# Optimization experiments

Measured on AMD Instinct MI355X. Metric: run time of the kernel, lower is better.

Reference implementation:

```python
import jax, jax.numpy as jnp
import numpy as np

N, E = 50000, 800000
F_NODE, F_EDGE, H, LAT, MAXN = 128, 16, 128, 64, 200


def setup_inputs() -> dict:
    key = jax.random.key(0)
    ks = jax.random.split(key, 40)
    s = 0.05
    p = {
        'x': jax.random.normal(ks[0], (N, F_NODE), jnp.float32),
        'edge_index': jax.random.randint(ks[1], (2, E), 0, N, jnp.int64),
        'edge_attr': jax.random.normal(ks[2], (E, F_EDGE), jnp.float32),
        'eps': jax.random.normal(ks[3], (1, LAT), jnp.float32),
        'num_nodes': N,
        # GATConv layer 1 (heads=1)
        'W1': jax.random.normal(ks[4], (F_NODE, H), jnp.float32) * s,
        'att_src1': jax.random.normal(ks[5], (H,), jnp.float32) * s,
        'att_dst1': jax.random.normal(ks[6], (H,), jnp.float32) * s,
        'We1': jax.random.normal(ks[7], (F_EDGE, H), jnp.float32) * s,
        'att_e1': jax.random.normal(ks[8], (H,), jnp.float32) * s,
        'b1': jnp.zeros((H,), jnp.float32),
        # GATConv layer 2
        'W2': jax.random.normal(ks[9], (H, H), jnp.float32) * s,
        'att_src2': jax.random.normal(ks[10], (H,), jnp.float32) * s,
        'att_dst2': jax.random.normal(ks[11], (H,), jnp.float32) * s,
        'We2': jax.random.normal(ks[12], (F_EDGE, H), jnp.float32) * s,
        'att_e2': jax.random.normal(ks[13], (H,), jnp.float32) * s,
        'b2': jnp.zeros((H,), jnp.float32),
        # heads
        'mu_W': jax.random.normal(ks[14], (H, LAT), jnp.float32) * s,
        'mu_b': jnp.zeros((LAT,), jnp.float32),
        'lv_W': jax.random.normal(ks[15], (H, LAT), jnp.float32) * s,
        'lv_b': jnp.zeros((LAT,), jnp.float32),
        'dec_W': jax.random.normal(ks[16], (LAT, H), jnp.float32) * s,
        'dec_b': jnp.zeros((H,), jnp.float32),
        'adj_W1': jax.random.normal(ks[17], (H, H), jnp.float32) * s,
        'adj_b1': jnp.zeros((H,), jnp.float32),
        'adj_W2': jax.random.normal(ks[18], (H, MAXN), jnp.float32) * s,
        'adj_b2': jnp.zeros((MAXN,), jnp.float32),
        'nd_W1': jax.random.normal(ks[19], (H, H), jnp.float32) * s,
        'nd_b1': jnp.zeros((H,), jnp.float32),
        'nd_W2': jax.random.normal(ks[20], (H, F_NODE), jnp.float32) * s,
        'nd_b2': jnp.zeros((F_NODE,), jnp.float32),
    }
    return p


def _gat(h, src, dst, ea, W, a_s, a_d, We, a_e, b, n):
    # PyG GATConv, heads=1: linear transform, per-edge attention, segment softmax over dst
    g = h @ W                                     # [n, H]
    alpha = jax.nn.leaky_relu((g @ a_s)[src] + (g @ a_d)[dst] + (ea @ We) @ a_e,
                              negative_slope=0.2)  # [E']
    m = jax.ops.segment_max(alpha, dst, num_segments=n)
    ex = jnp.exp(alpha - m[dst])
    den = jax.ops.segment_sum(ex, dst, num_segments=n)
    w = ex / den[dst]
    return jax.ops.segment_sum(w[:, None] * g[src], dst, num_segments=n) + b


def _forward(x, edge_index, edge_attr, eps, num_nodes,
             W1, att_src1, att_dst1, We1, att_e1, b1,
             W2, att_src2, att_dst2, We2, att_e2, b2,
             mu_W, mu_b, lv_W, lv_b, dec_W, dec_b,
             adj_W1, adj_b1, adj_W2, adj_b2, nd_W1, nd_b1, nd_W2, nd_b2):
    n = x.shape[0]
    src, dst = edge_index[0], edge_index[1]
    # add self loops; self-loop edge_attr = per-node mean of incoming edge_attr (PyG fill_value='mean')
    deg = jax.ops.segment_sum(jnp.ones((src.shape[0],), x.dtype), dst, num_segments=n)
    mean_ea = jax.ops.segment_sum(edge_attr, dst, num_segments=n) / jnp.maximum(deg, 1.0)[:, None]
    loop = jnp.arange(n)
    src_f = jnp.concatenate([src, loop])
    dst_f = jnp.concatenate([dst, loop])
    ea_f = jnp.concatenate([edge_attr, mean_ea])
    h = jax.nn.relu(_gat(x, src_f, dst_f, ea_f, W1, att_src1, att_dst1, We1, att_e1, b1, n))
    h = jax.nn.relu(_gat(h, src_f, dst_f, ea_f, W2, att_src2, att_dst2, We2, att_e2, b2, n))
    hg = h.mean(axis=0, keepdims=True)            # global_mean_pool, single graph -> [1, H]
    mu = hg @ mu_W + mu_b
    logvar = hg @ lv_W + lv_b
    z = mu + eps * jnp.exp(0.5 * logvar)
    hd = jax.nn.relu(z @ dec_W + dec_b)           # [1, H]
    hn = jnp.broadcast_to(hd[:, None, :], (1, num_nodes, hd.shape[-1]))
    adj = jax.nn.relu(hn @ adj_W1 + adj_b1) @ adj_W2 + adj_b2   # [1, n, MAXN]
    adj = adj[:, :, :num_nodes]
    nodes = jax.nn.relu(hn @ nd_W1 + nd_b1) @ nd_W2 + nd_b2     # [1, n, F_NODE]
    return adj, nodes, mu, logvar


def reference(x, edge_index, edge_attr, eps, num_nodes,
              W1, att_src1, att_dst1, We1, att_e1, b1,
              W2, att_src2, att_dst2, We2, att_e2, b2,
              mu_W, mu_b, lv_W, lv_b, dec_W, dec_b,
              adj_W1, adj_b1, adj_W2, adj_b2, nd_W1, nd_b1, nd_W2, nd_b2):
    return _forward(x, edge_index, edge_attr, eps, num_nodes,
                    W1, att_src1, att_dst1, We1, att_e1, b1,
                    W2, att_src2, att_dst2, We2, att_e2, b2,
                    mu_W, mu_b, lv_W, lv_b, dec_W, dec_b,
                    adj_W1, adj_b1, adj_W2, adj_b2, nd_W1, nd_b1, nd_W2, nd_b2)
```

## Files before the change

### kernel.cpp

```cpp
#include <hip/hip_runtime.h>
#include <math.h>

#define NN   50000
#define EE   800000
#define EF   850000
#define HH   128
#define FE   16
#define LATD 64
#define MAXNN 200

#define ADJ_TOT   10000000
#define NODES_TOT 6400000
#define OUT_TOT   16400000
#define MU_OFF    16400000
#define LV_OFF    16400064

#define GEMMBLOCKS 782
#define DEGBLOCKS  782
#define NBSCAN     49

typedef __attribute__((ext_vector_type(8))) short bf16x8;
typedef __attribute__((ext_vector_type(4))) float f32x4;
typedef __attribute__((ext_vector_type(2))) float f32x2;

__device__ __forceinline__ unsigned short f2bf(float f){
  unsigned int u = __float_as_uint(f);
  unsigned int r = (u + 0x7FFFu + ((u>>16)&1u)) >> 16;
  return (unsigned short)r;
}
__device__ __forceinline__ float bf2f(unsigned short h){
  return __uint_as_float(((unsigned int)h)<<16);
}

__device__ __forceinline__ void load_bo(const int* __restrict__ blocksum, int* bo, int tid){
  if(tid < 64){
    int v = (tid < NBSCAN)? blocksum[tid] : 0;
    int inc = v;
    #pragma unroll
    for(int off=1; off<64; off<<=1){
      int x = __shfl_up(inc, off);
      if(tid>=off) inc += x;
    }
    bo[tid] = inc - v;
  }
  __syncthreads();
}

__global__ __launch_bounds__(256) void kprep(int* ideg, float* hgsum,
                       const float* We1, const float* ae1, const float* We2, const float* ae2,
                       float* wa1, float* wa2,
                       const float* W1, const float* W2,
                       unsigned short* Wp1, unsigned short* Wp2){
  int i = blockIdx.x*256 + threadIdx.x;
  if(i < NN) ideg[i]=0;
  if(i < HH) hgsum[i]=0.f;
  if(i < FE){
    float s1=0.f, s2=0.f;
    for(int j=0;j<HH;j++){ s1 += We1[i*HH+j]*ae1[j]; s2 += We2[i*HH+j]*ae2[j]; }
    wa1[i]=s1; wa2[i]=s2;
  }
  if(i < HH*HH){
    int n = i >> 7, k = i & 127;
    Wp1[i] = f2bf(W1[k*HH + n]);
    Wp2[i] = f2bf(W2[k*HH + n]);
  }
}

__device__ __forceinline__ void gemm_body(int bid, int tid, const void* __restrict__ hin, int h_is_fp32,
    const unsigned short* __restrict__ Wp,
    const float* __restrict__ atts, const float* __restrict__ attd,
    unsigned char* __restrict__ A8, float* __restrict__ asrc, float* __restrict__ adst){
  int lane = tid & 63;
  int wid  = tid >> 6;
  int l = lane & 15, q = lane >> 4;
  int r0 = bid*64 + wid*16;
  if(r0 >= NN) return;
  const unsigned short* hb = (const unsigned short*)hin;
  const float*          hf = (const float*)hin;
  int row = r0 + l;

  bf16x8 afr[4];
  if(h_is_fp32){
    float4 u[8];
    #pragma unroll
    for(int kb=0;kb<4;kb++){
      const float* p = hf + (size_t)row*HH + kb*32 + q*8;
      u[kb*2]   = *(const float4*)(p);
      u[kb*2+1] = *(const float4*)(p+4);
    }
    #pragma unroll
    for(int kb=0;kb<4;kb++){
      afr[kb][0]=(short)f2bf(u[kb*2].x);   afr[kb][1]=(short)f2bf(u[kb*2].y);
      afr[kb][2]=(short)f2bf(u[kb*2].z);   afr[kb][3]=(short)f2bf(u[kb*2].w);
      afr[kb][4]=(short)f2bf(u[kb*2+1].x); afr[kb][5]=(short)f2bf(u[kb*2+1].y);
      afr[kb][6]=(short)f2bf(u[kb*2+1].z); afr[kb][7]=(short)f2bf(u[kb*2+1].w);
    }
  } else {
    #pragma unroll
    for(int kb=0;kb<4;kb++)
      afr[kb] = *(const bf16x8*)(hb + (size_t)row*HH + kb*32 + q*8);
  }

  f32x4 acc[8];
  #pragma unroll
  for(int t=0;t<8;t++) acc[t]=(f32x4){0.f,0.f,0.f,0.f};

  #pragma unroll
  for(int kb=0;kb<4;kb++){
    #pragma unroll
    for(int t=0;t<8;t++){
      bf16x8 b = *(const bf16x8*)(Wp + (size_t)(t*16+l)*HH + kb*32 + q*8);
      acc[t] = __builtin_amdgcn_mfma_f32_16x16x32_bf16(afr[kb], b, acc[t], 0,0,0);
    }
  }

  float av[8], dv[8];
  #pragma unroll
  for(int t=0;t<8;t++){ av[t]=atts[t*16+l]; dv[t]=attd[t*16+l]; }
  #pragma unroll
  for(int reg=0;reg<4;reg++){
    float ps=0.f, pd=0.f;
    #pragma unroll
    for(int t=0;t<8;t++){ ps+=acc[t][reg]*av[t]; pd+=acc[t][reg]*dv[t]; }
    #pragma unroll
    for(int m=8;m>=1;m>>=1){ ps+=__shfl_xor(ps,m,16); pd+=__shfl_xor(pd,m,16); }
    if(l==0){ int R=r0+q*4+reg; asrc[R]=ps; adst[R]=pd; }
  }
  #pragma unroll
  for(int t=0;t<8;t++)
    #pragma unroll
    for(int reg=0;reg<4;reg++){
      int pk = __builtin_amdgcn_cvt_pk_fp8_f32(acc[t][reg], 0.f, 0, false);
      A8[(size_t)(r0+q*4+reg)*HH + t*16 + l] = (unsigned char)(pk & 0xFF);
    }
}

__global__ __launch_bounds__(256) void kgemm3(const void* __restrict__ hin, int h_is_fp32,
    const unsigned short* __restrict__ Wp,
    const float* __restrict__ atts, const float* __restrict__ attd,
    unsigned char* __restrict__ A8, float* __restrict__ asrc, float* __restrict__ adst){
  gemm_body(blockIdx.x, threadIdx.x, hin, h_is_fp32, Wp, atts, attd, A8, asrc, adst);
}

__global__ __launch_bounds__(256) void kdeggemm(
    const int* __restrict__ ei, int* ideg, unsigned short* __restrict__ erank,
    const void* __restrict__ hin, int h_is_fp32,
    const unsigned short* __restrict__ Wp,
    const float* __restrict__ atts, const float* __restrict__ attd,
    unsigned char* __restrict__ A8, float* __restrict__ asrc, float* __restrict__ adst){
  if(blockIdx.x < GEMMBLOCKS){
    gemm_body(blockIdx.x, threadIdx.x, hin, h_is_fp32, Wp, atts, attd, A8, asrc, adst);
  } else {
    int e0 = ((blockIdx.x - GEMMBLOCKS)*256 + threadIdx.x)*4;
    if(e0 + 3 < EE){
      int4 d4 = *(const int4*)(ei + EE + e0);
      unsigned short r0 = (unsigned short)atomicAdd(&ideg[d4.x], 1);
      unsigned short r1 = (unsigned short)atomicAdd(&ideg[d4.y], 1);
      unsigned short r2 = (unsigned short)atomicAdd(&ideg[d4.z], 1);
      unsigned short r3 = (unsigned short)atomicAdd(&ideg[d4.w], 1);
      ushort4 rr; rr.x=r0; rr.y=r1; rr.z=r2; rr.w=r3;
      *(ushort4*)(erank + e0) = rr;
    } else {
      for(int j=0;j<4;j++)
        if(e0+j < EE) erank[e0+j] = (unsigned short)atomicAdd(&ideg[ei[EE+e0+j]], 1);
    }
  }
}

__global__ void kscan1(const int* __restrict__ ideg, int* rowstart, int* blocksum){
  __shared__ int sd[1024];
  int t=threadIdx.x; int i=blockIdx.x*1024+t;
  int v = (i<NN)? (ideg[i]+1) : 0;
  sd[t]=v; __syncthreads();
  for(int off=1; off<1024; off<<=1){
    int x = (t>=off)? sd[t-off] : 0;
    __syncthreads();
    sd[t] += x;
    __syncthreads();
  }
  if(i<NN) rowstart[i] = sd[t]-v;
  else if(i==NN) rowstart[NN] = sd[t];
  if(t==1023) blocksum[blockIdx.x]=sd[1023];
}

__device__ __forceinline__ unsigned etpack(const float4* a4,
                         const float* __restrict__ wa1, const float* __restrict__ wa2){
  float4 v0=a4[0], v1=a4[1], v2=a4[2], v3=a4[3];
  float va[16]={v0.x,v0.y,v0.z,v0.w, v1.x,v1.y,v1.z,v1.w,
                v2.x,v2.y,v2.z,v2.w, v3.x,v3.y,v3.z,v3.w};
  float d1=0.f,d2=0.f;
  #pragma unroll
  for(int f=0;f<FE;f++){ d1+=va[f]*wa1[f]; d2+=va[f]*wa2[f]; }
  return (unsigned)f2bf(d1) | ((unsigned)f2bf(d2)<<16);
}
__global__ __launch_bounds__(256) void kscatter(const int* __restrict__ ei, const float* __restrict__ ea,
                         const float* __restrict__ wa1, const float* __restrict__ wa2,
                         const int* __restrict__ rowstart, const int* __restrict__ blocksum,
                         const unsigned short* __restrict__ erank,
                         uint2* __restrict__ csr){
  __shared__ int bo[64];
  load_bo(blocksum, bo, threadIdx.x);
  int e0 = (blockIdx.x*256 + threadIdx.x)*2;
  if(e0>=EE) return;
  int sA=ei[e0],    sB=ei[e0+1];
  int dA=ei[EE+e0], dB=ei[EE+e0+1];
  int rA=(int)erank[e0], rB=(int)erank[e0+1];
  int pA=rowstart[dA]+bo[dA>>10]+rA, pB=rowstart[dB]+bo[dB>>10]+rB;
  const float4* a4 = (const float4*)(ea + (size_t)e0*FE);
  unsigned yA = etpack(a4,   wa1, wa2);
  unsigned yB = etpack(a4+4, wa1, wa2);
  uint2 enA; enA.x=(unsigned)sA; enA.y=yA;
  uint2 enB; enB.x=(unsigned)sB; enB.y=yB;
  csr[pA]=enA; csr[pB]=enB;
}

__global__ __launch_bounds__(256) void kgat(const unsigned char* __restrict__ A8,
    const float* __restrict__ asrc, const float* __restrict__ adst,
    const int* __restrict__ rowstart, const int* __restrict__ blocksum,
    const uint2* __restrict__ csr,
    int etsel, const float* __restrict__ bias,
    float* __restrict__ alphabuf, int* __restrict__ srcbuf,
    unsigned short* __restrict__ Bout){
  __shared__ int bo[64];
  load_bo(blocksum, bo, threadIdx.x);
  int lane = threadIdx.x & 63;
  int wid  = threadIdx.x >> 6;
  int i = blockIdx.x*4 + wid;
  if(i >= NN) return;
  int base = rowstart[i]   + bo[i>>10];
  int end  = rowstart[i+1] + bo[(i+1)>>10];
  int len  = end - base;
  float adi = adst[i];
  int lq = lane & 15;
  int qq = lane >> 4;
  float av[8];
  #pragma unroll
  for(int j=0;j<8;j++) av[j]=0.f;

  if(__builtin_expect(len <= 64, 1)){
    int s = i; float et = 0.f;
    if(lane < len-1){
      uint2 en = csr[base+lane];
      s = (int)en.x;
      et = etsel ? bf2f((unsigned short)(en.y>>16)) : bf2f((unsigned short)(en.y & 0xFFFFu));
    }
    float ets = (lane < len-1) ? et : 0.f;
    #pragma unroll
    for(int mk=32;mk>=1;mk>>=1) ets += __shfl_xor(ets,mk);
    if(lane == len-1) et = ets / fmaxf((float)(len-1), 1.f);
    float a = -1e30f;
    if(lane < len){
      a = asrc[s] + adi + et;
      a = fmaxf(a, 0.2f*a);
    }
    float m = a;
    #pragma unroll
    for(int mk=32;mk>=1;mk>>=1) m = fmaxf(m, __shfl_xor(m,mk));
    float ex = (lane<len) ? __expf(a-m) : 0.f;
    float sm = ex;
    #pragma unroll
    for(int mk=32;mk>=1;mk>>=1) sm += __shfl_xor(sm,mk);
    ex *= __builtin_amdgcn_rcpf(sm);

    int P4 = (len+3)>>2;
    for(int t0=0; t0<P4; t0+=6){
      int skv[6]; float w[6];
      #pragma unroll
      for(int j=0;j<6;j++){
        if(t0+j < P4){
          int idx = 4*(t0+j) + qq;
          skv[j] = __shfl(s, idx);
          w[j]   = __shfl(ex, idx);
        } else { skv[j] = i; w[j] = 0.f; }
      }
      unsigned ux[6], uy[6];
      #pragma unroll
      for(int j=0;j<6;j++){
        uint2 u = *(const uint2*)(A8 + (size_t)skv[j]*HH + lq*8);
        ux[j]=u.x; uy[j]=u.y;
      }
      #pragma unroll
      for(int j=0;j<6;j++){
        f32x2 v;
        v=__builtin_amdgcn_cvt_pk_f32_fp8((int)ux[j],false); av[0]+=w[j]*v[0]; av[1]+=w[j]*v[1];
        v=__builtin_amdgcn_cvt_pk_f32_fp8((int)ux[j],true ); av[2]+=w[j]*v[0]; av[3]+=w[j]*v[1];
        v=__builtin_amdgcn_cvt_pk_f32_fp8((int)uy[j],false); av[4]+=w[j]*v[0]; av[5]+=w[j]*v[1];
        v=__builtin_amdgcn_cvt_pk_f32_fp8((int)uy[j],true ); av[6]+=w[j]*v[0]; av[7]+=w[j]*v[1];
      }
    }
  } else {
    int deg = len-1;
    float lm = -1e30f, ets = 0.f;
    for(int k=lane;k<deg;k+=64){
      uint2 en = csr[base+k];
      int sr = (int)en.x;
      float et = etsel ? bf2f((unsigned short)(en.y>>16)) : bf2f((unsigned short)(en.y & 0xFFFFu));
      ets += et;
      float a = asrc[sr] + adi + et;
      a = fmaxf(a, 0.2f*a);
      alphabuf[base+k]=a; srcbuf[base+k]=sr;
      lm = fmaxf(lm,a);
    }
    #pragma unroll
    for(int mk=32;mk>=1;mk>>=1){
      ets += __shfl_xor(ets,mk);
      lm   = fmaxf(lm, __shfl_xor(lm,mk));
    }
    float aself = asrc[i] + adi + ets/(float)deg;
    aself = fmaxf(aself, 0.2f*aself);
    lm = fmaxf(lm, aself);
    float ls=0.f;
    for(int k=lane;k<len;k+=64){
      float a = (k<deg)? alphabuf[base+k] : aself;
      float e_ = __expf(a-lm);
      alphabuf[base+k]=e_;
      ls += e_;
    }
    #pragma unroll
    for(int mk=32;mk>=1;mk>>=1) ls += __shfl_xor(ls,mk);
    float inv = 1.f/ls;
    int P4 = (len+3)>>2;
    for(int t=0;t<P4;t++){
      int k = 4*t + qq;
      int sk = i; float wk = 0.f;
      if(k<len){
        sk = (k<deg)? srcbuf[base+k] : i;
        wk = alphabuf[base+k]*inv;
      }
      uint2 u = *(const uint2*)(A8 + (size_t)sk*HH + lq*8);
      f32x2 v;
      v=__builtin_amdgcn_cvt_pk_f32_fp8((int)u.x,false); av[0]+=wk*v[0]; av[1]+=wk*v[1];
      v=__builtin_amdgcn_cvt_pk_f32_fp8((int)u.x,true ); av[2]+=wk*v[0]; av[3]+=wk*v[1];
      v=__builtin_amdgcn_cvt_pk_f32_fp8((int)u.y,false); av[4]+=wk*v[0]; av[5]+=wk*v[1];
      v=__builtin_amdgcn_cvt_pk_f32_fp8((int)u.y,true ); av[6]+=wk*v[0]; av[7]+=wk*v[1];
    }
  }

  #pragma unroll
  for(int j=0;j<8;j++){
    av[j] += __shfl_xor(av[j],16);
    av[j] += __shfl_xor(av[j],32);
  }
  if(qq==0){
    const float4* bp = (const float4*)(bias + lq*8);
    float4 b0=bp[0], b1=bp[1];
    float o0=fmaxf(av[0]+b0.x,0.f), o1=fmaxf(av[1]+b0.y,0.f);
    float o2=fmaxf(av[2]+b0.z,0.f), o3=fmaxf(av[3]+b0.w,0.f);
    float o4=fmaxf(av[4]+b1.x,0.f), o5=fmaxf(av[5]+b1.y,0.f);
    float o6=fmaxf(av[6]+b1.z,0.f), o7=fmaxf(av[7]+b1.w,0.f);
    uint4 ov;
    ov.x=(unsigned)f2bf(o0)|((unsigned)f2bf(o1)<<16);
    ov.y=(unsigned)f2bf(o2)|((unsigned)f2bf(o3)<<16);
    ov.z=(unsigned)f2bf(o4)|((unsigned)f2bf(o5)<<16);
    ov.w=(unsigned)f2bf(o6)|((unsigned)f2bf(o7)<<16);
    *(uint4*)(Bout + (size_t)i*HH + lq*8) = ov;
  }
}

__global__ __launch_bounds__(256) void khg(const unsigned short* __restrict__ B, float* hgsum){
  int f = threadIdx.x & 127;
  int half = threadIdx.x >> 7;
  float s=0.f;
  for(int i = blockIdx.x*2+half; i < NN; i += gridDim.x*2)
    s += bf2f(B[(size_t)i*HH + f]);
  __shared__ float sd[256];
  sd[threadIdx.x]=s; __syncthreads();
  if(half==0) atomicAdd(&hgsum[f], sd[threadIdx.x]+sd[threadIdx.x+128]);
}

__global__ __launch_bounds__(256) void kdec(const float* __restrict__ hgsum, const float* __restrict__ eps,
   const float* muW,const float* mub,const float* lvW,const float* lvb,
   const float* decW,const float* decb,
   const float* aW1,const float* ab1,const float* aW2,const float* ab2,
   const float* nW1,const float* nb1,const float* nW2,const float* nb2,
   float* out, float* rowadj, float* rownodes){
  __shared__ float hg[HH], z[LATD], hd[HH], t1[HH], t2[HH];
  int t=threadIdx.x;
  if(t<HH) hg[t]=hgsum[t]*(1.0f/NN);
  __syncthreads();
  if(t<LATD){
    float mu=mub[t], lv=lvb[t];
    #pragma unroll 8
    for(int k=0;k<HH;k++){ mu += hg[k]*muW[k*LATD+t]; lv += hg[k]*lvW[k*LATD+t]; }
    out[MU_OFF+t]=mu; out[LV_OFF+t]=lv;
    z[t]=mu + eps[t]*expf(0.5f*lv);
  }
  __syncthreads();
  if(t<HH){
    float a=decb[t];
    #pragma unroll 8
    for(int k=0;k<LATD;k++) a += z[k]*decW[k*HH+t];
    hd[t]=fmaxf(a,0.f);
  }
  __syncthreads();
  if(t<HH){
    float a=ab1[t];
    #pragma unroll 8
    for(int k=0;k<HH;k++) a += hd[k]*aW1[k*HH+t];
    t1[t]=fmaxf(a,0.f);
  } else {
    int j=t-HH;
    float a=nb1[j];
    #pragma unroll 8
    for(int k=0;k<HH;k++) a += hd[k]*nW1[k*HH+j];
    t2[j]=fmaxf(a,0.f);
  }
  __syncthreads();
  for(int j=t;j<MAXNN;j+=256){
    float a=ab2[j];
    #pragma unroll 8
    for(int k=0;k<HH;k++) a += t1[k]*aW2[k*MAXNN+j];
    rowadj[j]=a;
  }
  if(t<HH){
    float a=nb2[t];
    #pragma unroll 8
    for(int k=0;k<HH;k++) a += t2[k]*nW2[k*HH+t];
    rownodes[t]=a;
  }
}

__global__ __launch_bounds__(256) void kbcast(const float* __restrict__ rowadj,
                                              const float* __restrict__ rownodes,
                                              float* __restrict__ out){
  __shared__ float row[MAXNN+HH];
  int t=threadIdx.x;
  if(t<MAXNN) row[t]=rowadj[t];
  if(t<HH) row[MAXNN+t]=rownodes[t];
  __syncthreads();
  int stride=gridDim.x*blockDim.x;
  const int tot4 = OUT_TOT/4;
  for(int q=blockIdx.x*blockDim.x+t; q<tot4; q+=stride){
    int idx = q*4;
    float4 vv;
    if(idx<ADJ_TOT){
      int j = idx % MAXNN;
      vv = *(const float4*)&row[j];
    } else {
      int j = (idx-ADJ_TOT) & (HH-1);
      vv = *(const float4*)&row[MAXNN+j];
    }
    *(float4*)&out[idx] = vv;
  }
}

extern "C" void kernel_launch(void* const* d_in, const int* in_sizes, int n_in,
                              void* d_out, int out_size, void* d_ws, size_t ws_size,
                              hipStream_t stream){
  const float* x   = (const float*)d_in[0];
  const int*   ei  = (const int*)d_in[1];
  const float* ea  = (const float*)d_in[2];
  const float* eps = (const float*)d_in[3];
  const float* W1  =(const float*)d_in[5];
  const float* as1 =(const float*)d_in[6];
  const float* ad1 =(const float*)d_in[7];
  const float* We1 =(const float*)d_in[8];
  const float* ae1 =(const float*)d_in[9];
  const float* b1  =(const float*)d_in[10];
  const float* W2  =(const float*)d_in[11];
  const float* as2 =(const float*)d_in[12];
  const float* ad2 =(const float*)d_in[13];
  const float* We2 =(const float*)d_in[14];
  const float* ae2 =(const float*)d_in[15];
  const float* b2  =(const float*)d_in[16];
  const float* muW =(const float*)d_in[17];
  const float* mub =(const float*)d_in[18];
  const float* lvW =(const float*)d_in[19];
  const float* lvb =(const float*)d_in[20];
  const float* decW=(const float*)d_in[21];
  const float* decb=(const float*)d_in[22];
  const float* aW1 =(const float*)d_in[23];
  const float* ab1 =(const float*)d_in[24];
  const float* aW2 =(const float*)d_in[25];
  const float* ab2 =(const float*)d_in[26];
  const float* nW1 =(const float*)d_in[27];
  const float* nb1 =(const float*)d_in[28];
  const float* nW2 =(const float*)d_in[29];
  const float* nb2 =(const float*)d_in[30];
  float* out=(float*)d_out;

  char* w=(char*)d_ws;
  unsigned char*  A8  = (unsigned char*)w;  w += (size_t)NN*HH;
  unsigned short* Bbf = (unsigned short*)w; w += (size_t)NN*HH*2;
  unsigned short* Wp1 = (unsigned short*)w; w += (size_t)HH*HH*2;
  unsigned short* Wp2 = (unsigned short*)w; w += (size_t)HH*HH*2;
  uint2*  csr      = (uint2*)w;  w += (size_t)EF*8;
  float*  alphabuf = (float*)w;  w += (size_t)EF*4;
  int*    srcbuf   = (int*)w;    w += (size_t)EF*4;
  unsigned short* erank = (unsigned short*)w; w += (size_t)EE*2;
  int*    rowstart = (int*)w;    w += (size_t)(NN+1)*4;
  int*    ideg     = (int*)w;    w += (size_t)NN*4;
  float*  hgsum    = (float*)w;  w += 128*4;
  float*  asrc     = (float*)w;  w += (size_t)NN*4;
  float*  adst     = (float*)w;  w += (size_t)NN*4;
  float*  wa1      = (float*)w;  w += 16*4;
  float*  wa2      = (float*)w;  w += 16*4;
  float*  rowadj   = (float*)w;  w += 256*4;
  float*  rownodes = (float*)w;  w += 128*4;
  int*    blocksum = (int*)w;    w += 64*4;

  int gatblocks  = (NN+3)/4;

  hipLaunchKernelGGL(kprep, dim3((NN+255)/256), dim3(256), 0, stream,
                     ideg, hgsum, We1, ae1, We2, ae2, wa1, wa2, W1, W2, Wp1, Wp2);
  hipLaunchKernelGGL(kdeggemm, dim3(GEMMBLOCKS+DEGBLOCKS), dim3(256), 0, stream,
                     ei, ideg, erank,
                     (const void*)x, 1, Wp1, as1, ad1, A8, asrc, adst);
  hipLaunchKernelGGL(kscan1, dim3(NBSCAN), dim3(1024), 0, stream, ideg, rowstart, blocksum);
  hipLaunchKernelGGL(kscatter, dim3((EE/2+255)/256), dim3(256), 0, stream,
                     ei, ea, wa1, wa2, rowstart, blocksum, erank, csr);
  hipLaunchKernelGGL(kgat,  dim3(gatblocks), dim3(256), 0, stream,
                     A8, asrc, adst, rowstart, blocksum, csr, 0, b1, alphabuf, srcbuf, Bbf);
  hipLaunchKernelGGL(kgemm3, dim3(GEMMBLOCKS), dim3(256), 0, stream,
                     (const void*)Bbf, 0, Wp2, as2, ad2, A8, asrc, adst);
  hipLaunchKernelGGL(kgat,  dim3(gatblocks), dim3(256), 0, stream,
                     A8, asrc, adst, rowstart, blocksum, csr, 1, b2, alphabuf, srcbuf, Bbf);
  hipLaunchKernelGGL(khg,   dim3(512), dim3(256), 0, stream, Bbf, hgsum);
  hipLaunchKernelGGL(kdec,  dim3(1), dim3(256), 0, stream, hgsum, eps,
                     muW,mub,lvW,lvb,decW,decb,aW1,ab1,aW2,ab2,nW1,nb1,nW2,nb2,
                     out, rowadj, rownodes);
  hipLaunchKernelGGL(kbcast, dim3(2048), dim3(256), 0, stream, rowadj, rownodes, out);
}
```

Measured before the change: 412.5 us.

## Move edge-attr projection into deg/gemm kernel, vectorize scatter, prefetch first gather batch

The per-edge attention projection of edge_attr moves out of the scatter kernel into extra blocks of the fused degree/GEMM kernel. There it writes a packed ety buffer and overlaps with the GEMM and atomics instead of sitting on the serial scan→scatter path. The scatter now handles 4 edges per thread with vector loads. In the GAT kernel, the first batch of A8 row gathers is issued before the softmax reductions to hide their latency. The cost is an extra 3.2MB write and read of ety, plus more live registers in kgat.

```diff
diff --git a/kernel.cpp b/kernel.cpp
--- a/kernel.cpp
+++ b/kernel.cpp
@@ -17,6 +17,7 @@
 
 #define GEMMBLOCKS 782
 #define DEGBLOCKS  782
+#define EPBLOCKS   1563
 #define NBSCAN     49
 
 typedef __attribute__((ext_vector_type(8))) short bf16x8;
@@ -142,15 +143,28 @@
   gemm_body(blockIdx.x, threadIdx.x, hin, h_is_fp32, Wp, atts, attd, A8, asrc, adst);
 }
 
+__device__ __forceinline__ unsigned etpack(const float4* a4,
+                         const float* __restrict__ wa1, const float* __restrict__ wa2){
+  float4 v0=a4[0], v1=a4[1], v2=a4[2], v3=a4[3];
+  float va[16]={v0.x,v0.y,v0.z,v0.w, v1.x,v1.y,v1.z,v1.w,
+                v2.x,v2.y,v2.z,v2.w, v3.x,v3.y,v3.z,v3.w};
+  float d1=0.f,d2=0.f;
+  #pragma unroll
+  for(int f=0;f<FE;f++){ d1+=va[f]*wa1[f]; d2+=va[f]*wa2[f]; }
+  return (unsigned)f2bf(d1) | ((unsigned)f2bf(d2)<<16);
+}
+
 __global__ __launch_bounds__(256) void kdeggemm(
     const int* __restrict__ ei, int* ideg, unsigned short* __restrict__ erank,
+    const float* __restrict__ ea, const float* __restrict__ wa1, const float* __restrict__ wa2,
+    unsigned* __restrict__ ety,
     const void* __restrict__ hin, int h_is_fp32,
     const unsigned short* __restrict__ Wp,
     const float* __restrict__ atts, const float* __restrict__ attd,
     unsigned char* __restrict__ A8, float* __restrict__ asrc, float* __restrict__ adst){
   if(blockIdx.x < GEMMBLOCKS){
     gemm_body(blockIdx.x, threadIdx.x, hin, h_is_fp32, Wp, atts, attd, A8, asrc, adst);
-  } else {
+  } else if(blockIdx.x < GEMMBLOCKS+DEGBLOCKS){
     int e0 = ((blockIdx.x - GEMMBLOCKS)*256 + threadIdx.x)*4;
     if(e0 + 3 < EE){
       int4 d4 = *(const int4*)(ei + EE + e0);
@@ -164,6 +178,14 @@
       for(int j=0;j<4;j++)
         if(e0+j < EE) erank[e0+j] = (unsigned short)atomicAdd(&ideg[ei[EE+e0+j]], 1);
     }
+  } else {
+    int e0 = ((blockIdx.x - GEMMBLOCKS - DEGBLOCKS)*256 + threadIdx.x)*2;
+    if(e0 >= EE) return;
+    const float4* a4 = (const float4*)(ea + (size_t)e0*FE);
+    uint2 y;
+    y.x = etpack(a4,   wa1, wa2);
+    y.y = etpack(a4+4, wa1, wa2);
+    *(uint2*)(ety + e0) = y;
   }
 }
 
@@ -183,35 +205,34 @@
   if(t==1023) blocksum[blockIdx.x]=sd[1023];
 }
 
-__device__ __forceinline__ unsigned etpack(const float4* a4,
-                         const float* __restrict__ wa1, const float* __restrict__ wa2){
-  float4 v0=a4[0], v1=a4[1], v2=a4[2], v3=a4[3];
-  float va[16]={v0.x,v0.y,v0.z,v0.w, v1.x,v1.y,v1.z,v1.w,
-                v2.x,v2.y,v2.z,v2.w, v3.x,v3.y,v3.z,v3.w};
-  float d1=0.f,d2=0.f;
-  #pragma unroll
-  for(int f=0;f<FE;f++){ d1+=va[f]*wa1[f]; d2+=va[f]*wa2[f]; }
-  return (unsigned)f2bf(d1) | ((unsigned)f2bf(d2)<<16);
-}
-__global__ __launch_bounds__(256) void kscatter(const int* __restrict__ ei, const float* __restrict__ ea,
-                         const float* __restrict__ wa1, const float* __restrict__ wa2,
+__global__ __launch_bounds__(256) void kscatter(const int* __restrict__ ei,
+                         const unsigned* __restrict__ ety,
                          const int* __restrict__ rowstart, const int* __restrict__ blocksum,
                          const unsigned short* __restrict__ erank,
                          uint2* __restrict__ csr){
   __shared__ int bo[64];
   load_bo(blocksum, bo, threadIdx.x);
-  int e0 = (blockIdx.x*256 + threadIdx.x)*2;
-  if(e0>=EE) return;
-  int sA=ei[e0],    sB=ei[e0+1];
-  int dA=ei[EE+e0], dB=ei[EE+e0+1];
-  int rA=(int)erank[e0], rB=(int)erank[e0+1];
-  int pA=rowstart[dA]+bo[dA>>10]+rA, pB=rowstart[dB]+bo[dB>>10]+rB;
-  const float4* a4 = (const float4*)(ea + (size_t)e0*FE);
-  unsigned yA = etpack(a4,   wa1, wa2);
-  unsigned yB = etpack(a4+4, wa1, wa2);
-  uint2 enA; enA.x=(unsigned)sA; enA.y=yA;
-  uint2 enB; enB.x=(unsigned)sB; enB.y=yB;
-  csr[pA]=enA; csr[pB]=enB;
+  int e0 = (blockIdx.x*256 + threadIdx.x)*4;
+  if(e0+3 < EE){
+    int4 s4 = *(const int4*)(ei + e0);
+    int4 d4 = *(const int4*)(ei + EE + e0);
+    ushort4 r4 = *(const ushort4*)(erank + e0);
+    uint4 y4 = *(const uint4*)(ety + e0);
+    uint2 en;
+    en.x=(unsigned)s4.x; en.y=y4.x; csr[rowstart[d4.x]+bo[d4.x>>10]+(int)r4.x]=en;
+    en.x=(unsigned)s4.y; en.y=y4.y; csr[rowstart[d4.y]+bo[d4.y>>10]+(int)r4.y]=en;
+    en.x=(unsigned)s4.z; en.y=y4.z; csr[rowstart[d4.z]+bo[d4.z>>10]+(int)r4.z]=en;
+    en.x=(unsigned)s4.w; en.y=y4.w; csr[rowstart[d4.w]+bo[d4.w>>10]+(int)r4.w]=en;
+  } else {
+    for(int j=0;j<4;j++){
+      int e=e0+j;
+      if(e<EE){
+        int s=ei[e], d=ei[EE+e];
+        uint2 en; en.x=(unsigned)s; en.y=ety[e];
+        csr[rowstart[d]+bo[d>>10]+(int)erank[e]]=en;
+      }
+    }
+  }
 }
 
 __global__ __launch_bounds__(256) void kgat(const unsigned char* __restrict__ A8,
@@ -238,11 +259,21 @@
   for(int j=0;j<8;j++) av[j]=0.f;
 
   if(__builtin_expect(len <= 64, 1)){
+    int P4 = (len+3)>>2;
     int s = i; float et = 0.f;
     if(lane < len-1){
       uint2 en = csr[base+lane];
       s = (int)en.x;
       et = etsel ? bf2f((unsigned short)(en.y>>16)) : bf2f((unsigned short)(en.y & 0xFFFFu));
+    }
+    int skv0[6];
+    #pragma unroll
+    for(int j=0;j<6;j++) skv0[j] = (j<P4) ? __shfl(s, 4*j+qq) : i;
+    unsigned ux[6], uy[6];
+    #pragma unroll
+    for(int j=0;j<6;j++){
+      uint2 u = *(const uint2*)(A8 + (size_t)skv0[j]*HH + lq*8);
+      ux[j]=u.x; uy[j]=u.y;
     }
     float ets = (lane < len-1) ? et : 0.f;
     #pragma unroll
@@ -262,8 +293,18 @@
     for(int mk=32;mk>=1;mk>>=1) sm += __shfl_xor(sm,mk);
     ex *= __builtin_amdgcn_rcpf(sm);
 
-    int P4 = (len+3)>>2;
-    for(int t0=0; t0<P4; t0+=6){
+    float w0[6];
+    #pragma unroll
+    for(int j=0;j<6;j++) w0[j] = (j<P4) ? __shfl(ex, 4*j+qq) : 0.f;
+    #pragma unroll
+    for(int j=0;j<6;j++){
+      f32x2 v;
+      v=__builtin_amdgcn_cvt_pk_f32_fp8((int)ux[j],false); av[0]+=w0[j]*v[0]; av[1]+=w0[j]*v[1];
+      v=__builtin_amdgcn_cvt_pk_f32_fp8((int)ux[j],true ); av[2]+=w0[j]*v[0]; av[3]+=w0[j]*v[1];
+      v=__builtin_amdgcn_cvt_pk_f32_fp8((int)uy[j],false); av[4]+=w0[j]*v[0]; av[5]+=w0[j]*v[1];
+      v=__builtin_amdgcn_cvt_pk_f32_fp8((int)uy[j],true ); av[6]+=w0[j]*v[0]; av[7]+=w0[j]*v[1];
+    }
+    for(int t0=6; t0<P4; t0+=6){
       int skv[6]; float w[6];
       #pragma unroll
       for(int j=0;j<6;j++){
@@ -273,19 +314,19 @@
           w[j]   = __shfl(ex, idx);
         } else { skv[j] = i; w[j] = 0.f; }
       }
-      unsigned ux[6], uy[6];
+      unsigned vx[6], vy[6];
       #pragma unroll
       for(int j=0;j<6;j++){
         uint2 u = *(const uint2*)(A8 + (size_t)skv[j]*HH + lq*8);
-        ux[j]=u.x; uy[j]=u.y;
+        vx[j]=u.x; vy[j]=u.y;
       }
       #pragma unroll
       for(int j=0;j<6;j++){
         f32x2 v;
-        v=__builtin_amdgcn_cvt_pk_f32_fp8((int)ux[j],false); av[0]+=w[j]*v[0]; av[1]+=w[j]*v[1];
-        v=__builtin_amdgcn_cvt_pk_f32_fp8((int)ux[j],true ); av[2]+=w[j]*v[0]; av[3]+=w[j]*v[1];
-        v=__builtin_amdgcn_cvt_pk_f32_fp8((int)uy[j],false); av[4]+=w[j]*v[0]; av[5]+=w[j]*v[1];
-        v=__builtin_amdgcn_cvt_pk_f32_fp8((int)uy[j],true ); av[6]+=w[j]*v[0]; av[7]+=w[j]*v[1];
+        v=__builtin_amdgcn_cvt_pk_f32_fp8((int)vx[j],false); av[0]+=w[j]*v[0]; av[1]+=w[j]*v[1];
+        v=__builtin_amdgcn_cvt_pk_f32_fp8((int)vx[j],true ); av[2]+=w[j]*v[0]; av[3]+=w[j]*v[1];
+        v=__builtin_amdgcn_cvt_pk_f32_fp8((int)vy[j],false); av[4]+=w[j]*v[0]; av[5]+=w[j]*v[1];
+        v=__builtin_amdgcn_cvt_pk_f32_fp8((int)vy[j],true ); av[6]+=w[j]*v[0]; av[7]+=w[j]*v[1];
       }
     }
   } else {
@@ -487,6 +528,7 @@
   uint2*  csr      = (uint2*)w;  w += (size_t)EF*8;
   float*  alphabuf = (float*)w;  w += (size_t)EF*4;
   int*    srcbuf   = (int*)w;    w += (size_t)EF*4;
+  unsigned* ety    = (unsigned*)w; w += (size_t)EE*4;
   unsigned short* erank = (unsigned short*)w; w += (size_t)EE*2;
   int*    rowstart = (int*)w;    w += (size_t)(NN+1)*4;
   int*    ideg     = (int*)w;    w += (size_t)NN*4;
@@ -503,12 +545,12 @@
 
   hipLaunchKernelGGL(kprep, dim3((NN+255)/256), dim3(256), 0, stream,
                      ideg, hgsum, We1, ae1, We2, ae2, wa1, wa2, W1, W2, Wp1, Wp2);
-  hipLaunchKernelGGL(kdeggemm, dim3(GEMMBLOCKS+DEGBLOCKS), dim3(256), 0, stream,
-                     ei, ideg, erank,
+  hipLaunchKernelGGL(kdeggemm, dim3(GEMMBLOCKS+DEGBLOCKS+EPBLOCKS), dim3(256), 0, stream,
+                     ei, ideg, erank, ea, wa1, wa2, ety,
                      (const void*)x, 1, Wp1, as1, ad1, A8, asrc, adst);
   hipLaunchKernelGGL(kscan1, dim3(NBSCAN), dim3(1024), 0, stream, ideg, rowstart, blocksum);
-  hipLaunchKernelGGL(kscatter, dim3((EE/2+255)/256), dim3(256), 0, stream,
-                     ei, ea, wa1, wa2, rowstart, blocksum, erank, csr);
+  hipLaunchKernelGGL(kscatter, dim3((EE/4+255)/256), dim3(256), 0, stream,
+                     ei, ety, rowstart, blocksum, erank, csr);
   hipLaunchKernelGGL(kgat,  dim3(gatblocks), dim3(256), 0, stream,
                      A8, asrc, adst, rowstart, blocksum, csr, 0, b1, alphabuf, srcbuf, Bbf);
   hipLaunchKernelGGL(kgemm3, dim3(GEMMBLOCKS), dim3(256), 0, stream,
```

After: 415.9 us. About the same (+0.8%).

## Finalize rowstart offsets once, cache self-loop attrs in CSR, fuse decoder with broadcast

Applied to the files above, without the earlier changes.

A new small kernel adds the scan block offsets into rowstart once, so kscatter and kgat no longer rebuild the offset table in every block. The first GAT pass writes the self-loop mean edge attention for both layers into the CSR slot, and the second pass just reads it, which removes that reduction. The first batch of neighbor feature gathers is issued before the softmax so its latency overlaps the math. The decoder and broadcast are merged into one 512-block kernel in which every block recomputes the tiny MLP redundantly. This saves a launch but repeats a small amount of work in each block.

```diff
diff --git a/kernel.cpp b/kernel.cpp
--- a/kernel.cpp
+++ b/kernel.cpp
@@ -30,20 +30,6 @@
 }
 __device__ __forceinline__ float bf2f(unsigned short h){
   return __uint_as_float(((unsigned int)h)<<16);
-}
-
-__device__ __forceinline__ void load_bo(const int* __restrict__ blocksum, int* bo, int tid){
-  if(tid < 64){
-    int v = (tid < NBSCAN)? blocksum[tid] : 0;
-    int inc = v;
-    #pragma unroll
-    for(int off=1; off<64; off<<=1){
-      int x = __shfl_up(inc, off);
-      if(tid>=off) inc += x;
-    }
-    bo[tid] = inc - v;
-  }
-  __syncthreads();
 }
 
 __global__ __launch_bounds__(256) void kprep(int* ideg, float* hgsum,
@@ -179,8 +165,25 @@
     __syncthreads();
   }
   if(i<NN) rowstart[i] = sd[t]-v;
-  else if(i==NN) rowstart[NN] = sd[t];
   if(t==1023) blocksum[blockIdx.x]=sd[1023];
+}
+__global__ __launch_bounds__(256) void kscan3i(int* rowstart, const int* __restrict__ blocksum){
+  __shared__ int bo[64];
+  int t = threadIdx.x;
+  if(t < 64){
+    int v = (t < NBSCAN)? blocksum[t] : 0;
+    int inc = v;
+    #pragma unroll
+    for(int off=1; off<64; off<<=1){
+      int x = __shfl_up(inc, off);
+      if(t>=off) inc += x;
+    }
+    bo[t] = inc - v;
+  }
+  __syncthreads();
+  int i = blockIdx.x*256 + t;
+  if(i<NN) rowstart[i] += bo[i>>10];
+  if(i==0) rowstart[NN] = bo[NBSCAN];
 }
 
 __device__ __forceinline__ unsigned etpack(const float4* a4,
@@ -195,17 +198,14 @@
 }
 __global__ __launch_bounds__(256) void kscatter(const int* __restrict__ ei, const float* __restrict__ ea,
                          const float* __restrict__ wa1, const float* __restrict__ wa2,
-                         const int* __restrict__ rowstart, const int* __restrict__ blocksum,
-                         const unsigned short* __restrict__ erank,
+                         const int* __restrict__ rowstart, const unsigned short* __restrict__ erank,
                          uint2* __restrict__ csr){
-  __shared__ int bo[64];
-  load_bo(blocksum, bo, threadIdx.x);
   int e0 = (blockIdx.x*256 + threadIdx.x)*2;
   if(e0>=EE) return;
   int sA=ei[e0],    sB=ei[e0+1];
   int dA=ei[EE+e0], dB=ei[EE+e0+1];
   int rA=(int)erank[e0], rB=(int)erank[e0+1];
-  int pA=rowstart[dA]+bo[dA>>10]+rA, pB=rowstart[dB]+bo[dB>>10]+rB;
+  int pA=rowstart[dA]+rA, pB=rowstart[dB]+rB;
   const float4* a4 = (const float4*)(ea + (size_t)e0*FE);
   unsigned yA = etpack(a4,   wa1, wa2);
   unsigned yB = etpack(a4+4, wa1, wa2);
@@ -216,20 +216,16 @@
 
 __global__ __launch_bounds__(256) void kgat(const unsigned char* __restrict__ A8,
     const float* __restrict__ asrc, const float* __restrict__ adst,
-    const int* __restrict__ rowstart, const int* __restrict__ blocksum,
-    const uint2* __restrict__ csr,
-    int etsel, const float* __restrict__ bias,
+    const int* __restrict__ rowstart, uint2* __restrict__ csr,
+    int mode, const float* __restrict__ bias,
     float* __restrict__ alphabuf, int* __restrict__ srcbuf,
     unsigned short* __restrict__ Bout){
-  __shared__ int bo[64];
-  load_bo(blocksum, bo, threadIdx.x);
   int lane = threadIdx.x & 63;
   int wid  = threadIdx.x >> 6;
   int i = blockIdx.x*4 + wid;
   if(i >= NN) return;
-  int base = rowstart[i]   + bo[i>>10];
-  int end  = rowstart[i+1] + bo[(i+1)>>10];
-  int len  = end - base;
+  int base = rowstart[i];
+  int len  = rowstart[i+1]-base;
   float adi = adst[i];
   int lq = lane & 15;
   int qq = lane >> 4;
@@ -238,16 +234,39 @@
   for(int j=0;j<8;j++) av[j]=0.f;
 
   if(__builtin_expect(len <= 64, 1)){
-    int s = i; float et = 0.f;
-    if(lane < len-1){
+    int P4 = (len+3)>>2;
+    int nread = mode ? len : len-1;
+    int s = i; float etlo = 0.f, ethi = 0.f;
+    if(lane < nread){
       uint2 en = csr[base+lane];
       s = (int)en.x;
-      et = etsel ? bf2f((unsigned short)(en.y>>16)) : bf2f((unsigned short)(en.y & 0xFFFFu));
-    }
-    float ets = (lane < len-1) ? et : 0.f;
-    #pragma unroll
-    for(int mk=32;mk>=1;mk>>=1) ets += __shfl_xor(ets,mk);
-    if(lane == len-1) et = ets / fmaxf((float)(len-1), 1.f);
+      etlo = bf2f((unsigned short)(en.y & 0xFFFFu));
+      ethi = bf2f((unsigned short)(en.y >> 16));
+    }
+    float et = mode ? ethi : etlo;
+    int skv0[6];
+    #pragma unroll
+    for(int j=0;j<6;j++) skv0[j] = (j<P4) ? __shfl(s, 4*j+qq) : i;
+    unsigned ux[6], uy[6];
+    #pragma unroll
+    for(int j=0;j<6;j++){
+      uint2 u = *(const uint2*)(A8 + (size_t)skv0[j]*HH + lq*8);
+      ux[j]=u.x; uy[j]=u.y;
+    }
+    if(!mode){
+      float e1 = (lane < len-1) ? etlo : 0.f;
+      float e2 = (lane < len-1) ? ethi : 0.f;
+      #pragma unroll
+      for(int mk=32;mk>=1;mk>>=1){ e1 += __shfl_xor(e1,mk); e2 += __shfl_xor(e2,mk); }
+      float dg = fmaxf((float)(len-1), 1.f);
+      float m1 = e1/dg, m2 = e2/dg;
+      if(lane == len-1){
+        et = m1;
+        uint2 se; se.x=(unsigned)i;
+        se.y=(unsigned)f2bf(m1) | ((unsigned)f2bf(m2)<<16);
+        csr[base+len-1] = se;
+      }
+    }
     float a = -1e30f;
     if(lane < len){
       a = asrc[s] + adi + et;
@@ -262,8 +281,18 @@
     for(int mk=32;mk>=1;mk>>=1) sm += __shfl_xor(sm,mk);
     ex *= __builtin_amdgcn_rcpf(sm);
 
-    int P4 = (len+3)>>2;
-    for(int t0=0; t0<P4; t0+=6){
+    float w0[6];
+    #pragma unroll
+    for(int j=0;j<6;j++) w0[j] = (j<P4) ? __shfl(ex, 4*j+qq) : 0.f;
+    #pragma unroll
+    for(int j=0;j<6;j++){
+      f32x2 v;
+      v=__builtin_amdgcn_cvt_pk_f32_fp8((int)ux[j],false); av[0]+=w0[j]*v[0]; av[1]+=w0[j]*v[1];
+      v=__builtin_amdgcn_cvt_pk_f32_fp8((int)ux[j],true ); av[2]+=w0[j]*v[0]; av[3]+=w0[j]*v[1];
+      v=__builtin_amdgcn_cvt_pk_f32_fp8((int)uy[j],false); av[4]+=w0[j]*v[0]; av[5]+=w0[j]*v[1];
+      v=__builtin_amdgcn_cvt_pk_f32_fp8((int)uy[j],true ); av[6]+=w0[j]*v[0]; av[7]+=w0[j]*v[1];
+    }
+    for(int t0=6; t0<P4; t0+=6){
       int skv[6]; float w[6];
       #pragma unroll
       for(int j=0;j<6;j++){
@@ -273,45 +302,60 @@
           w[j]   = __shfl(ex, idx);
         } else { skv[j] = i; w[j] = 0.f; }
       }
-      unsigned ux[6], uy[6];
+      unsigned vx[6], vy[6];
       #pragma unroll
       for(int j=0;j<6;j++){
         uint2 u = *(const uint2*)(A8 + (size_t)skv[j]*HH + lq*8);
-        ux[j]=u.x; uy[j]=u.y;
+        vx[j]=u.x; vy[j]=u.y;
       }
       #pragma unroll
       for(int j=0;j<6;j++){
         f32x2 v;
-        v=__builtin_amdgcn_cvt_pk_f32_fp8((int)ux[j],false); av[0]+=w[j]*v[0]; av[1]+=w[j]*v[1];
-        v=__builtin_amdgcn_cvt_pk_f32_fp8((int)ux[j],true ); av[2]+=w[j]*v[0]; av[3]+=w[j]*v[1];
-        v=__builtin_amdgcn_cvt_pk_f32_fp8((int)uy[j],false); av[4]+=w[j]*v[0]; av[5]+=w[j]*v[1];
-        v=__builtin_amdgcn_cvt_pk_f32_fp8((int)uy[j],true ); av[6]+=w[j]*v[0]; av[7]+=w[j]*v[1];
+        v=__builtin_amdgcn_cvt_pk_f32_fp8((int)vx[j],false); av[0]+=w[j]*v[0]; av[1]+=w[j]*v[1];
+        v=__builtin_amdgcn_cvt_pk_f32_fp8((int)vx[j],true ); av[2]+=w[j]*v[0]; av[3]+=w[j]*v[1];
+        v=__builtin_amdgcn_cvt_pk_f32_fp8((int)vy[j],false); av[4]+=w[j]*v[0]; av[5]+=w[j]*v[1];
+        v=__builtin_amdgcn_cvt_pk_f32_fp8((int)vy[j],true ); av[6]+=w[j]*v[0]; av[7]+=w[j]*v[1];
       }
     }
   } else {
     int deg = len-1;
-    float lm = -1e30f, ets = 0.f;
-    for(int k=lane;k<deg;k+=64){
+    int lim = mode ? len : deg;
+    float lm = -1e30f, e1 = 0.f, e2 = 0.f;
+    for(int k=lane;k<lim;k+=64){
       uint2 en = csr[base+k];
       int sr = (int)en.x;
-      float et = etsel ? bf2f((unsigned short)(en.y>>16)) : bf2f((unsigned short)(en.y & 0xFFFFu));
-      ets += et;
-      float a = asrc[sr] + adi + et;
+      float lo = bf2f((unsigned short)(en.y & 0xFFFFu));
+      float hi = bf2f((unsigned short)(en.y >> 16));
+      float etv = mode ? hi : lo;
+      if(!mode){ e1 += lo; e2 += hi; }
+      float a = asrc[sr] + adi + etv;
       a = fmaxf(a, 0.2f*a);
       alphabuf[base+k]=a; srcbuf[base+k]=sr;
       lm = fmaxf(lm,a);
     }
     #pragma unroll
     for(int mk=32;mk>=1;mk>>=1){
-      ets += __shfl_xor(ets,mk);
-      lm   = fmaxf(lm, __shfl_xor(lm,mk));
-    }
-    float aself = asrc[i] + adi + ets/(float)deg;
-    aself = fmaxf(aself, 0.2f*aself);
-    lm = fmaxf(lm, aself);
+      e1 += __shfl_xor(e1,mk);
+      e2 += __shfl_xor(e2,mk);
+      lm  = fmaxf(lm, __shfl_xor(lm,mk));
+    }
+    float aself = 0.f;
+    if(!mode){
+      float m1 = e1/(float)deg, m2 = e2/(float)deg;
+      aself = asrc[i] + adi + m1;
+      aself = fmaxf(aself, 0.2f*aself);
+      lm = fmaxf(lm, aself);
+      if(lane==0){
+        uint2 se; se.x=(unsigned)i;
+        se.y=(unsigned)f2bf(m1) | ((unsigned)f2bf(m2)<<16);
+        csr[base+deg] = se;
+      }
+    }
     float ls=0.f;
     for(int k=lane;k<len;k+=64){
-      float a = (k<deg)? alphabuf[base+k] : aself;
+      float a;
+      if(mode) a = alphabuf[base+k];
+      else     a = (k<deg)? alphabuf[base+k] : aself;
       float e_ = __expf(a-lm);
       alphabuf[base+k]=e_;
       ls += e_;
@@ -319,12 +363,13 @@
     #pragma unroll
     for(int mk=32;mk>=1;mk>>=1) ls += __shfl_xor(ls,mk);
     float inv = 1.f/ls;
+    int lim2 = mode ? len : deg;
     int P4 = (len+3)>>2;
     for(int t=0;t<P4;t++){
       int k = 4*t + qq;
       int sk = i; float wk = 0.f;
       if(k<len){
-        sk = (k<deg)? srcbuf[base+k] : i;
+        sk = (k<lim2)? srcbuf[base+k] : i;
         wk = alphabuf[base+k]*inv;
       }
       uint2 u = *(const uint2*)(A8 + (size_t)sk*HH + lq*8);
@@ -368,13 +413,14 @@
   if(half==0) atomicAdd(&hgsum[f], sd[threadIdx.x]+sd[threadIdx.x+128]);
 }
 
-__global__ __launch_bounds__(256) void kdec(const float* __restrict__ hgsum, const float* __restrict__ eps,
+__global__ __launch_bounds__(256) void kdecbcast(const float* __restrict__ hgsum, const float* __restrict__ eps,
    const float* muW,const float* mub,const float* lvW,const float* lvb,
    const float* decW,const float* decb,
    const float* aW1,const float* ab1,const float* aW2,const float* ab2,
    const float* nW1,const float* nb1,const float* nW2,const float* nb2,
-   float* out, float* rowadj, float* rownodes){
+   float* __restrict__ out){
   __shared__ float hg[HH], z[LATD], hd[HH], t1[HH], t2[HH];
+  __shared__ float row[MAXNN+HH];
   int t=threadIdx.x;
   if(t<HH) hg[t]=hgsum[t]*(1.0f/NN);
   __syncthreads();
@@ -382,7 +428,7 @@
     float mu=mub[t], lv=lvb[t];
     #pragma unroll 8
     for(int k=0;k<HH;k++){ mu += hg[k]*muW[k*LATD+t]; lv += hg[k]*lvW[k*LATD+t]; }
-    out[MU_OFF+t]=mu; out[LV_OFF+t]=lv;
+    if(blockIdx.x==0){ out[MU_OFF+t]=mu; out[LV_OFF+t]=lv; }
     z[t]=mu + eps[t]*expf(0.5f*lv);
   }
   __syncthreads();
@@ -410,23 +456,14 @@
     float a=ab2[j];
     #pragma unroll 8
     for(int k=0;k<HH;k++) a += t1[k]*aW2[k*MAXNN+j];
-    rowadj[j]=a;
+    row[j]=a;
   }
   if(t<HH){
     float a=nb2[t];
     #pragma unroll 8
     for(int k=0;k<HH;k++) a += t2[k]*nW2[k*HH+t];
-    rownodes[t]=a;
-  }
-}
-
-__global__ __launch_bounds__(256) void kbcast(const float* __restrict__ rowadj,
-                                              const float* __restrict__ rownodes,
-                                              float* __restrict__ out){
-  __shared__ float row[MAXNN+HH];
-  int t=threadIdx.x;
-  if(t<MAXNN) row[t]=rowadj[t];
-  if(t<HH) row[MAXNN+t]=rownodes[t];
+    row[MAXNN+t]=a;
+  }
   __syncthreads();
   int stride=gridDim.x*blockDim.x;
   const int tot4 = OUT_TOT/4;
@@ -495,8 +532,6 @@
   float*  adst     = (float*)w;  w += (size_t)NN*4;
   float*  wa1      = (float*)w;  w += 16*4;
   float*  wa2      = (float*)w;  w += 16*4;
-  float*  rowadj   = (float*)w;  w += 256*4;
-  float*  rownodes = (float*)w;  w += 128*4;
   int*    blocksum = (int*)w;    w += 64*4;
 
   int gatblocks  = (NN+3)/4;
@@ -507,17 +542,17 @@
                      ei, ideg, erank,
                      (const void*)x, 1, Wp1, as1, ad1, A8, asrc, adst);
   hipLaunchKernelGGL(kscan1, dim3(NBSCAN), dim3(1024), 0, stream, ideg, rowstart, blocksum);
+  hipLaunchKernelGGL(kscan3i, dim3((NN+255)/256), dim3(256), 0, stream, rowstart, blocksum);
   hipLaunchKernelGGL(kscatter, dim3((EE/2+255)/256), dim3(256), 0, stream,
-                     ei, ea, wa1, wa2, rowstart, blocksum, erank, csr);
+                     ei, ea, wa1, wa2, rowstart, erank, csr);
   hipLaunchKernelGGL(kgat,  dim3(gatblocks), dim3(256), 0, stream,
-                     A8, asrc, adst, rowstart, blocksum, csr, 0, b1, alphabuf, srcbuf, Bbf);
+                     A8, asrc, adst, rowstart, csr, 0, b1, alphabuf, srcbuf, Bbf);
   hipLaunchKernelGGL(kgemm3, dim3(GEMMBLOCKS), dim3(256), 0, stream,
                      (const void*)Bbf, 0, Wp2, as2, ad2, A8, asrc, adst);
   hipLaunchKernelGGL(kgat,  dim3(gatblocks), dim3(256), 0, stream,
-                     A8, asrc, adst, rowstart, blocksum, csr, 1, b2, alphabuf, srcbuf, Bbf);
+                     A8, asrc, adst, rowstart, csr, 1, b2, alphabuf, srcbuf, Bbf);
   hipLaunchKernelGGL(khg,   dim3(512), dim3(256), 0, stream, Bbf, hgsum);
-  hipLaunchKernelGGL(kdec,  dim3(1), dim3(256), 0, stream, hgsum, eps,
+  hipLaunchKernelGGL(kdecbcast, dim3(512), dim3(256), 0, stream, hgsum, eps,
                      muW,mub,lvW,lvb,decW,decb,aW1,ab1,aW2,ab2,nW1,nb1,nW2,nb2,
-                     out, rowadj, rownodes);
-  hipLaunchKernelGGL(kbcast, dim3(2048), dim3(256), 0, stream, rowadj, rownodes, out);
-}
+                     out);
+}
```

Measured after the change: 408.6 us. No clear change (-0.9%).
